# Optimization experiments

Measured on AMD Instinct MI355X. Metric: run time of the kernel, lower is better.

The kernel has to match this reference:

```python
import jax, jax.numpy as jnp
import numpy as np
import math
from jax import lax

B, C, L = 8, 512, 1024
NCONV, K, H = 4, 7, 8
DH = C // H
EPS = 1e-5
NEG = -1e30


def layer_norm(x, g, b):
    mu = jnp.mean(x, axis=-1, keepdims=True)
    var = jnp.mean(jnp.square(x - mu), axis=-1, keepdims=True)
    return (x - mu) * lax.rsqrt(var + EPS) * g + b


def positional_encoding(d, n):
    pos = jnp.arange(n, dtype=jnp.float32)[:, None]                     # [n,1]
    div = jnp.exp(jnp.arange(0, d, 2, dtype=jnp.float32) * (-math.log(10000.0) / d))
    ang = pos * div                                                      # [n,d/2]
    pe = jnp.zeros((d, n), dtype=jnp.float32)
    pe = pe.at[0::2].set(jnp.sin(ang).T).at[1::2].set(jnp.cos(ang).T)
    return pe                                                            # [d,n]


def setup_inputs() -> dict:
    key = jax.random.key(0)
    ks = jax.random.split(key, 20)
    s = 0.02
    inp = {
        "x": jax.random.normal(ks[0], (B, C, L), jnp.float32),
        "mask": jnp.ones((B, L), jnp.float32),
        # conv stack params (stacked over NCONV layers)
        "dw_w": jax.random.normal(ks[1], (NCONV, C, 1, K), jnp.float32) * s,
        "dw_b": jnp.zeros((NCONV, C), jnp.float32),
        "pw_w": jax.random.normal(ks[2], (NCONV, C, C), jnp.float32) * s,
        "pw_b": jnp.zeros((NCONV, C), jnp.float32),
        "ln_conv_g": jnp.ones((NCONV, C), jnp.float32),
        "ln_conv_b": jnp.zeros((NCONV, C), jnp.float32),
        # attention params (torch Linear layout: [out,in])
        "Wq": jax.random.normal(ks[3], (C, C), jnp.float32) * s,
        "bq": jnp.zeros((C,), jnp.float32),
        "Wk": jax.random.normal(ks[4], (C, C), jnp.float32) * s,
        "bk": jnp.zeros((C,), jnp.float32),
        "Wv": jax.random.normal(ks[5], (C, C), jnp.float32) * s,
        "bv": jnp.zeros((C,), jnp.float32),
        "Wo": jax.random.normal(ks[6], (C, C), jnp.float32) * s,
        "bo": jnp.zeros((C,), jnp.float32),
        "ln_att_g": jnp.ones((C,), jnp.float32),
        "ln_att_b": jnp.zeros((C,), jnp.float32),
        # final fc + its layernorm
        "Wf": jax.random.normal(ks[7], (C, C), jnp.float32) * s,
        "bf": jnp.zeros((C,), jnp.float32),
        "ln_fc_g": jnp.ones((C,), jnp.float32),
        "ln_fc_b": jnp.zeros((C,), jnp.float32),
    }
    return inp


def reference(x, mask, dw_w, dw_b, pw_w, pw_b, ln_conv_g, ln_conv_b,
              Wq, bq, Wk, bk, Wv, bv, Wo, bo, ln_att_g, ln_att_b,
              Wf, bf, ln_fc_g, ln_fc_b):
    # positional encoding on channels-first input, then -> [B,L,C]
    out = x + positional_encoding(C, L)[None]          # [B,C,L]; dropout = eval mode (identity)
    out = out.transpose(0, 2, 1)                       # [B,L,C]
    res = out
    for i in range(NCONV):                             # fixed small layer loop
        h = layer_norm(out, ln_conv_g[i], ln_conv_b[i])
        h = h.transpose(0, 2, 1)                       # [B,C,L]
        h = lax.conv_general_dilated(h, dw_w[i], (1,), [(K // 2, K // 2)],
                                     dimension_numbers=("NCH", "OIH", "NCH"),
                                     feature_group_count=C) + dw_b[i][None, :, None]
        h = jnp.einsum("bcl,oc->bol", h, pw_w[i]) + pw_b[i][None, :, None]
        h = jax.nn.relu(h).transpose(0, 2, 1)          # [B,L,C]
        out = h + res
        res = out
    # masked multi-head self-attention
    a = layer_norm(out, ln_att_g, ln_att_b)
    q = (a @ Wq.T + bq).reshape(B, L, H, DH)
    k = (a @ Wk.T + bk).reshape(B, L, H, DH)
    v = (a @ Wv.T + bv).reshape(B, L, H, DH)
    scale = 1.0 / math.sqrt(DH)
    scores = jnp.einsum("blhd,bmhd->bhlm", q, k) * scale   # [B,H,L,L]
    m = mask[:, None, None, :]                              # mask over keys
    scores = scores * m + (1.0 - m) * NEG
    attn = jax.nn.softmax(scores, axis=-1)
    o = jnp.einsum("bhlm,bmhd->blhd", attn, v).reshape(B, L, C)
    o = o @ Wo.T + bo
    out = o + res
    res = out
    # feed-forward (single Linear + relu) with residual
    f = layer_norm(out, ln_fc_g, ln_fc_b)
    f = jax.nn.relu(f @ Wf.T + bf)
    out = f + res
    return out
```

## Files before the change

kernel.cpp:

```cpp
#include <hip/hip_runtime.h>
#include <hip/hip_bf16.h>

#define L_SEQ 1024
#define CCH   512
#define NB    8

typedef __bf16 bf16_t;
typedef __bf16 bf16x4 __attribute__((ext_vector_type(4)));
typedef __bf16 bf16x8 __attribute__((ext_vector_type(8)));
typedef float  f32x4  __attribute__((ext_vector_type(4)));

__device__ __forceinline__ void gload_lds16(const void* g, void* l) {
  __builtin_amdgcn_global_load_lds((const __attribute__((address_space(1))) void*)g,
                                   (__attribute__((address_space(3))) void*)l, 16, 0, 0);
}

__global__ __launch_bounds__(256) void cvtall_kernel(
    const float* __restrict__ pw_w, const float* __restrict__ Wq,
    const float* __restrict__ Wk, const float* __restrict__ Wv,
    const float* __restrict__ Wo, const float* __restrict__ Wf,
    const float* __restrict__ dw_w,
    bf16_t* __restrict__ WPW, bf16_t* __restrict__ WQKV,
    bf16_t* __restrict__ WOB, bf16_t* __restrict__ WFB,
    float* __restrict__ WT) {
  int idx = blockIdx.x * 256 + threadIdx.x;
  if (idx < 1048576) { WPW[idx] = (bf16_t)pw_w[idx]; return; }
  idx -= 1048576;
  if (idx < 262144) { WQKV[idx] = (bf16_t)Wq[idx]; return; }
  idx -= 262144;
  if (idx < 262144) { WQKV[262144 + idx] = (bf16_t)Wk[idx]; return; }
  idx -= 262144;
  if (idx < 262144) { WQKV[524288 + idx] = (bf16_t)Wv[idx]; return; }
  idx -= 262144;
  if (idx < 262144) { WOB[idx] = (bf16_t)Wo[idx]; return; }
  idx -= 262144;
  if (idx < 262144) { WFB[idx] = (bf16_t)Wf[idx]; return; }
  idx -= 262144;
  if (idx < 14336) {
    int i = idx / 3584, r = idx % 3584, t = r >> 9, c = r & 511;
    WT[idx] = dw_w[i * 3584 + c * 7 + t];
  }
}

__global__ __launch_bounds__(256) void pet_kernel(float* __restrict__ PET) {
  int idx = blockIdx.x * 256 + threadIdx.x;
  int l = idx >> 9, c = idx & 511;
  float div = expf(-(float)(2 * (c >> 1)) * (9.210340371976184f / 512.0f));
  float ang = (float)l * div;
  PET[idx] = (c & 1) ? cosf(ang) : sinf(ang);
}

__global__ __launch_bounds__(256) void pe_kernel(const float* __restrict__ x,
                                                 const float* __restrict__ PET,
                                                 float* __restrict__ out) {
  __shared__ float tile[32][33];
  int l0 = blockIdx.x * 32, c0 = blockIdx.y * 32, b = blockIdx.z;
  int tx = threadIdx.x, ty = threadIdx.y;
#pragma unroll
  for (int r = 0; r < 32; r += 8)
    tile[ty + r][tx] = x[(size_t)(b * CCH + c0 + ty + r) * L_SEQ + l0 + tx];
  __syncthreads();
#pragma unroll
  for (int r = 0; r < 32; r += 8) {
    int l = l0 + ty + r, c = c0 + tx;
    out[(size_t)(b * L_SEQ + l) * CCH + c] = tile[tx][ty + r] + PET[l * CCH + c];
  }
}

__global__ __launch_bounds__(256) void stats_kernel(const float* __restrict__ in,
                                                    float* __restrict__ Psum,
                                                    float* __restrict__ Psq) {
  int w = threadIdx.x >> 6, l = threadIdx.x & 63;
  int row = blockIdx.x * 4 + w;
  const float* p = in + (size_t)row * CCH + l * 8;
  float v[8];
  *(float4*)(&v[0]) = *(const float4*)p;
  *(float4*)(&v[4]) = *(const float4*)(p + 4);
  float s = 0.f, q = 0.f;
#pragma unroll
  for (int j = 0; j < 8; j++) { s += v[j]; q += v[j] * v[j]; }
  s += __shfl_xor(s, 1); q += __shfl_xor(q, 1);
  s += __shfl_xor(s, 2); q += __shfl_xor(q, 2);
  s += __shfl_xor(s, 4); q += __shfl_xor(q, 4);
  if ((l & 7) == 0) {
    Psum[row * 8 + (l >> 3)] = s;
    Psq[row * 8 + (l >> 3)] = q;
  }
}

__global__ __launch_bounds__(256) void ln_apply_kernel(const float* __restrict__ in,
                                                       const float* __restrict__ Psum,
                                                       const float* __restrict__ Psq,
                                                       const float* __restrict__ gam,
                                                       const float* __restrict__ bet,
                                                       bf16_t* __restrict__ out) {
  int w = threadIdx.x >> 6, l = threadIdx.x & 63;
  int row = blockIdx.x * 4 + w;
  float v0 = 0.f;
  if (l < 8) v0 = Psum[row * 8 + l];
  else if (l < 16) v0 = Psq[row * 8 + (l - 8)];
  v0 += __shfl_xor(v0, 1); v0 += __shfl_xor(v0, 2); v0 += __shfl_xor(v0, 4);
  float sum = __shfl(v0, 0), sq = __shfl(v0, 8);
  float mean = sum * (1.0f / 512.0f);
  float var = sq * (1.0f / 512.0f) - mean * mean;
  float inv = rsqrtf(var + 1e-5f);
  const float* p = in + (size_t)row * CCH + l * 8;
  float v[8], gv[8], bv[8];
  *(float4*)(&v[0]) = *(const float4*)p;
  *(float4*)(&v[4]) = *(const float4*)(p + 4);
  *(float4*)(&gv[0]) = *(const float4*)(gam + l * 8);
  *(float4*)(&gv[4]) = *(const float4*)(gam + l * 8 + 4);
  *(float4*)(&bv[0]) = *(const float4*)(bet + l * 8);
  *(float4*)(&bv[4]) = *(const float4*)(bet + l * 8 + 4);
  bf16x8 o;
#pragma unroll
  for (int j = 0; j < 8; j++) o[j] = (bf16_t)((v[j] - mean) * inv * gv[j] + bv[j]);
  *(bf16x8*)(out + (size_t)row * CCH + l * 8) = o;
}

__global__ __launch_bounds__(256) void dwln_kernel(const float* __restrict__ in,
                                                   const float* __restrict__ Psum,
                                                   const float* __restrict__ Psq,
                                                   const float* __restrict__ gam,
                                                   const float* __restrict__ bet,
                                                   const float* __restrict__ wtt,
                                                   const float* __restrict__ dbias,
                                                   bf16_t* __restrict__ out) {
  int idx = blockIdx.x * 256 + threadIdx.x;
  int lane = threadIdx.x & 63;
  int row = idx >> 6;
  int l = row & (L_SEQ - 1);
  float m_ = 0.f, i_ = 0.f;
  if (lane < 7) {
    int ll = l + lane - 3;
    if (ll >= 0 && ll < L_SEQ) {
      int rr = row + lane - 3;
      float s = 0.f, q = 0.f;
#pragma unroll
      for (int c = 0; c < 8; c++) { s += Psum[rr * 8 + c]; q += Psq[rr * 8 + c]; }
      float mm = s * (1.0f / 512.0f);
      m_ = mm;
      i_ = rsqrtf(q * (1.0f / 512.0f) - mm * mm + 1e-5f);
    }
  }
  float gv[8], bv[8], acc[8];
  *(float4*)&gv[0] = *(const float4*)(gam + lane * 8);
  *(float4*)&gv[4] = *(const float4*)(gam + lane * 8 + 4);
  *(float4*)&bv[0] = *(const float4*)(bet + lane * 8);
  *(float4*)&bv[4] = *(const float4*)(bet + lane * 8 + 4);
  *(float4*)&acc[0] = *(const float4*)(dbias + lane * 8);
  *(float4*)&acc[4] = *(const float4*)(dbias + lane * 8 + 4);
#pragma unroll
  for (int t = 0; t < 7; t++) {
    float mt = __shfl(m_, t), it = __shfl(i_, t);
    int ll = l + t - 3;
    if (ll >= 0 && ll < L_SEQ) {
      const float* p = in + (size_t)(row + t - 3) * CCH + lane * 8;
      float v[8], wv[8];
      *(float4*)&v[0] = *(const float4*)p;
      *(float4*)&v[4] = *(const float4*)(p + 4);
      *(float4*)&wv[0] = *(const float4*)(wtt + t * CCH + lane * 8);
      *(float4*)&wv[4] = *(const float4*)(wtt + t * CCH + lane * 8 + 4);
#pragma unroll
      for (int j = 0; j < 8; j++)
        acc[j] += ((v[j] - mt) * it * gv[j] + bv[j]) * wv[j];
    }
  }
  bf16x8 o;
#pragma unroll
  for (int j = 0; j < 8; j++) o[j] = (bf16_t)acc[j];
  *(bf16x8*)&out[(size_t)row * CCH + lane * 8] = o;
}

#define GEMM_STAGE(SRCA, SRCB, BI, K0)                                            \
  do {                                                                            \
    _Pragma("unroll") for (int cc = 0; cc < 2; cc++) {                            \
      int row_ = cc * 32 + w * 8 + srow;                                          \
      int off_ = (scb ^ ((row_ & 7) << 4)) >> 1;                                  \
      gload_lds16(SRCA + (size_t)(m0 + row_) * CCH + (K0) + off_,                 \
                  &As[BI][(cc * 32 + w * 8) * 64]);                               \
    }                                                                             \
    _Pragma("unroll") for (int cc = 0; cc < 4; cc++) {                            \
      int row_ = cc * 32 + w * 8 + srow;                                          \
      int off_ = (scb ^ ((row_ & 7) << 4)) >> 1;                                  \
      gload_lds16(SRCB + (size_t)(n0 + row_) * CCH + (K0) + off_,                 \
                  &Bs[BI][(cc * 32 + w * 8) * 64]);                               \
    }                                                                             \
  } while (0)

#define GEMM_COMPUTE(BI)                                                          \
  do {                                                                            \
    _Pragma("unroll") for (int ks = 0; ks < 2; ks++) {                            \
      bf16x8 fa[2], fb[4];                                                        \
      _Pragma("unroll") for (int i = 0; i < 2; i++) {                             \
        int ra = wr * 32 + i * 16 + lc;                                           \
        fa[i] = *(const bf16x8*)&As[BI][ra * 64 +                                 \
                 (((ks * 64 + lg * 16) ^ ((ra & 7) << 4)) >> 1)];                 \
      }                                                                           \
      _Pragma("unroll") for (int j = 0; j < 4; j++) {                             \
        int rb = wc * 64 + j * 16 + lc;                                           \
        fb[j] = *(const bf16x8*)&Bs[BI][rb * 64 +                                 \
                 (((ks * 64 + lg * 16) ^ ((rb & 7) << 4)) >> 1)];                 \
      }                                                                           \
      _Pragma("unroll") for (int i = 0; i < 2; i++)                               \
        _Pragma("unroll") for (int j = 0; j < 4; j++)                             \
          acc[i][j] = __builtin_amdgcn_mfma_f32_16x16x32_bf16(fa[i], fb[j],       \
                                                              acc[i][j], 0, 0, 0);\
    }                                                                             \
  } while (0)

template <int RELU, int RES, int BF16OUT, int STATS>
__global__ __launch_bounds__(256) void gemm_kernel(const bf16_t* __restrict__ A,
                                                   const bf16_t* __restrict__ W,
                                                   const float* __restrict__ bias,
                                                   const float* __restrict__ res,
                                                   float* __restrict__ outf,
                                                   bf16_t* __restrict__ outb,
                                                   float* __restrict__ Psum,
                                                   float* __restrict__ Psq) {
  __shared__ __align__(16) bf16_t As[2][64 * 64];
  __shared__ __align__(16) bf16_t Bs[2][128 * 64];
  int tid = threadIdx.x;
  int w = tid >> 6, l = tid & 63;
  int m0 = blockIdx.x * 64, n0 = blockIdx.y * 128;
  int wr = w >> 1, wc = w & 1;
  int lc = l & 15, lg = l >> 4;
  int srow = l >> 3, scb = (l & 7) * 16;
  f32x4 acc[2][4];
#pragma unroll
  for (int i = 0; i < 2; i++)
#pragma unroll
    for (int j = 0; j < 4; j++) acc[i][j] = f32x4{0.f, 0.f, 0.f, 0.f};

  GEMM_STAGE(A, W, 0, 0);
  __syncthreads();
  int cur = 0;
  for (int t = 0; t < 8; t++) {
    if (t < 7) GEMM_STAGE(A, W, cur ^ 1, (t + 1) * 64);
    GEMM_COMPUTE(cur);
    __syncthreads();
    cur ^= 1;
  }

  float ps[2][4], pq[2][4];
  if (STATS) {
#pragma unroll
    for (int i = 0; i < 2; i++)
#pragma unroll
      for (int r = 0; r < 4; r++) { ps[i][r] = 0.f; pq[i][r] = 0.f; }
  }
#pragma unroll
  for (int i = 0; i < 2; i++) {
    int mbase = m0 + wr * 32 + i * 16 + lg * 4;
#pragma unroll
    for (int j = 0; j < 4; j++) {
      int n = n0 + wc * 64 + j * 16 + lc;
      float bn = bias[n];
#pragma unroll
      for (int r = 0; r < 4; r++) {
        int m = mbase + r;
        float v2 = acc[i][j][r] + bn;
        if (RELU) v2 = fmaxf(v2, 0.f);
        if (RES) v2 += res[(size_t)m * CCH + n];
        if (BF16OUT) outb[(size_t)m * CCH + n] = (bf16_t)v2;
        else outf[(size_t)m * CCH + n] = v2;
        if (STATS) { ps[i][r] += v2; pq[i][r] += v2 * v2; }
      }
    }
  }
  if (STATS) {
    int chunk = blockIdx.y * 2 + wc;
#pragma unroll
    for (int i = 0; i < 2; i++)
#pragma unroll
      for (int r = 0; r < 4; r++) {
        float s = ps[i][r], q = pq[i][r];
        s += __shfl_xor(s, 1); q += __shfl_xor(q, 1);
        s += __shfl_xor(s, 2); q += __shfl_xor(q, 2);
        s += __shfl_xor(s, 4); q += __shfl_xor(q, 4);
        s += __shfl_xor(s, 8); q += __shfl_xor(q, 8);
        if (lc == 0) {
          int row = m0 + wr * 32 + i * 16 + lg * 4 + r;
          Psum[row * 8 + chunk] = s;
          Psq[row * 8 + chunk] = q;
        }
      }
  }
}

__global__ __launch_bounds__(256) void qkv_kernel(const bf16_t* __restrict__ A,
                                                  const bf16_t* __restrict__ Wqkv,
                                                  const float* __restrict__ bq,
                                                  const float* __restrict__ bk,
                                                  const float* __restrict__ bv,
                                                  bf16_t* __restrict__ QB,
                                                  bf16_t* __restrict__ KB,
                                                  bf16_t* __restrict__ VT) {
  __shared__ __align__(16) bf16_t As[2][64 * 64];
  __shared__ __align__(16) bf16_t Bs[2][128 * 64];
  int tid = threadIdx.x;
  int w = tid >> 6, l = tid & 63;
  int m0 = blockIdx.x * 64, n0 = blockIdx.y * 128;
  int sec = n0 >> 9;
  int wr = w >> 1, wc = w & 1;
  int lc = l & 15, lg = l >> 4;
  int srow = l >> 3, scb = (l & 7) * 16;
  f32x4 acc[2][4];
#pragma unroll
  for (int i = 0; i < 2; i++)
#pragma unroll
    for (int j = 0; j < 4; j++) acc[i][j] = f32x4{0.f, 0.f, 0.f, 0.f};

  GEMM_STAGE(A, Wqkv, 0, 0);
  __syncthreads();
  int cur = 0;
  for (int t = 0; t < 8; t++) {
    if (t < 7) GEMM_STAGE(A, Wqkv, cur ^ 1, (t + 1) * 64);
    GEMM_COMPUTE(cur);
    __syncthreads();
    cur ^= 1;
  }

  const float* bp = (sec == 0) ? bq : (sec == 1) ? bk : bv;
#pragma unroll
  for (int i = 0; i < 2; i++) {
    int mbase = m0 + wr * 32 + i * 16 + lg * 4;
#pragma unroll
    for (int j = 0; j < 4; j++) {
      int n = n0 + wc * 64 + j * 16 + lc;
      int nl = n & 511;
      float bn = bp[nl];
      if (sec < 2) {
        bf16_t* ob = (sec == 0) ? QB : KB;
#pragma unroll
        for (int r = 0; r < 4; r++)
          ob[(size_t)(mbase + r) * CCH + nl] = (bf16_t)(acc[i][j][r] + bn);
      } else {
        int h = nl >> 6, d = nl & 63;
        int b = mbase >> 10, lpos = mbase & 1023;
        bf16x4 t;
#pragma unroll
        for (int r = 0; r < 4; r++) t[r] = (bf16_t)(acc[i][j][r] + bn);
        *(bf16x4*)&VT[(((size_t)(b * 8 + h) * 64 + d) * L_SEQ) + lpos] = t;
      }
    }
  }
}

__global__ __launch_bounds__(256) void attn_kernel(const bf16_t* __restrict__ Q,
                                                   const bf16_t* __restrict__ K,
                                                   const bf16_t* __restrict__ VT,
                                                   const float* __restrict__ mask,
                                                   bf16_t* __restrict__ O) {
  __shared__ __align__(16) bf16_t Ks[64 * 64];
  __shared__ __align__(16) bf16_t Vs[64 * 64];
  __shared__ __align__(16) bf16_t Pl[4][16 * 64];
  int tid = threadIdx.x;
  int w = tid >> 6, l = tid & 63;
  int bid = blockIdx.x;
  int sw = (bid & 7) * 128 + (bid >> 3);
  int qb = sw & 15, h = (sw >> 4) & 7, b = sw >> 7;
  int lg = l >> 4, lc = l & 15;

  int qrow = qb * 64 + w * 16 + lc;
  const bf16_t* qptr = Q + ((size_t)(b * L_SEQ + qrow) * CCH + h * 64);
  bf16x8 qf0 = *(const bf16x8*)(qptr + lg * 8);
  bf16x8 qf1 = *(const bf16x8*)(qptr + 32 + lg * 8);

  f32x4 oacc[4];
  float psl[4] = {0.f, 0.f, 0.f, 0.f};
#pragma unroll
  for (int nf = 0; nf < 4; nf++) oacc[nf] = f32x4{0.f, 0.f, 0.f, 0.f};

  int srow = l >> 3;
  int scb = (l & 7) * 16;

  for (int kc = 0; kc < 16; kc++) {
#pragma unroll
    for (int r = 0; r < 2; r++) {
      int row = r * 32 + w * 8 + srow;
      int sc = (scb ^ ((row & 7) << 4)) >> 1;
      int key = kc * 64 + row;
      gload_lds16(K + ((size_t)(b * L_SEQ + key) * CCH + h * 64 + sc),
                  &Ks[(r * 32 + w * 8) * 64]);
      gload_lds16(VT + (((size_t)(b * 8 + h) * 64 + row) * L_SEQ + kc * 64 + sc),
                  &Vs[(r * 32 + w * 8) * 64]);
    }
    __syncthreads();

    f32x4 sacc[4];
#pragma unroll
    for (int kf = 0; kf < 4; kf++) sacc[kf] = f32x4{0.f, 0.f, 0.f, 0.f};
#pragma unroll
    for (int kf = 0; kf < 4; kf++) {
      int row = kf * 16 + lc;
      int s = (row & 7) << 4;
      const bf16_t* kr = &Ks[row * 64];
      bf16x8 b0 = *(const bf16x8*)(kr + (((lg * 16) ^ s) >> 1));
      sacc[kf] = __builtin_amdgcn_mfma_f32_16x16x32_bf16(qf0, b0, sacc[kf], 0, 0, 0);
      bf16x8 b1 = *(const bf16x8*)(kr + (((64 + lg * 16) ^ s) >> 1));
      sacc[kf] = __builtin_amdgcn_mfma_f32_16x16x32_bf16(qf1, b1, sacc[kf], 0, 0, 0);
    }

#pragma unroll
    for (int kf = 0; kf < 4; kf++) {
      float mv = mask[b * L_SEQ + kc * 64 + kf * 16 + lc];
      float mneg = (1.f - mv) * (-1e30f);
      float msc = 0.125f * mv;
#pragma unroll
      for (int j = 0; j < 4; j++) {
        float p = __expf(sacc[kf][j] * msc + mneg);
        psl[j] += p;
        int q = lg * 4 + j;
        int cb = (kf * 32 + lc * 2) ^ ((q & 7) << 4);
        Pl[w][(q * 128 + cb) >> 1] = (bf16_t)p;
      }
    }

    int sp = (lc & 7) << 4;
    bf16x8 pa0 = *(const bf16x8*)&Pl[w][(lc * 128 + ((lg * 16) ^ sp)) >> 1];
    bf16x8 pa1 = *(const bf16x8*)&Pl[w][(lc * 128 + ((64 + lg * 16) ^ sp)) >> 1];
#pragma unroll
    for (int nf = 0; nf < 4; nf++) {
      int d = nf * 16 + lc;
      int s = (d & 7) << 4;
      const bf16_t* vr = &Vs[d * 64];
      bf16x8 vb0 = *(const bf16x8*)(vr + (((lg * 16) ^ s) >> 1));
      oacc[nf] = __builtin_amdgcn_mfma_f32_16x16x32_bf16(pa0, vb0, oacc[nf], 0, 0, 0);
      bf16x8 vb1 = *(const bf16x8*)(vr + (((64 + lg * 16) ^ s) >> 1));
      oacc[nf] = __builtin_amdgcn_mfma_f32_16x16x32_bf16(pa1, vb1, oacc[nf], 0, 0, 0);
    }
    __syncthreads();
  }

#pragma unroll
  for (int off = 1; off < 16; off <<= 1)
#pragma unroll
    for (int j = 0; j < 4; j++) psl[j] += __shfl_xor(psl[j], off);

#pragma unroll
  for (int j = 0; j < 4; j++) {
    float is = 1.0f / psl[j];
    int r = qb * 64 + w * 16 + lg * 4 + j;
    bf16_t* op = O + ((size_t)(b * L_SEQ + r) * CCH + h * 64);
#pragma unroll
    for (int nf = 0; nf < 4; nf++) op[nf * 16 + lc] = (bf16_t)(oacc[nf][j] * is);
  }
}

extern "C" void kernel_launch(void* const* d_in, const int* in_sizes, int n_in,
                              void* d_out, int out_size, void* d_ws, size_t ws_size,
                              hipStream_t stream) {
  const float* x = (const float*)d_in[0];
  const float* mask = (const float*)d_in[1];
  const float* dw_w = (const float*)d_in[2];
  const float* dw_b = (const float*)d_in[3];
  const float* pw_w = (const float*)d_in[4];
  const float* pw_b = (const float*)d_in[5];
  const float* ln_conv_g = (const float*)d_in[6];
  const float* ln_conv_b = (const float*)d_in[7];
  const float* Wq = (const float*)d_in[8];  const float* bq = (const float*)d_in[9];
  const float* Wk = (const float*)d_in[10]; const float* bk = (const float*)d_in[11];
  const float* Wv = (const float*)d_in[12]; const float* bv = (const float*)d_in[13];
  const float* Wo = (const float*)d_in[14]; const float* bo = (const float*)d_in[15];
  const float* ln_att_g = (const float*)d_in[16]; const float* ln_att_b = (const float*)d_in[17];
  const float* Wf = (const float*)d_in[18]; const float* bfc = (const float*)d_in[19];
  const float* ln_fc_g = (const float*)d_in[20]; const float* ln_fc_b = (const float*)d_in[21];

  float* OUT = (float*)d_out;

  char* ws = (char*)d_ws;
  bf16_t* ABF  = (bf16_t*)(ws);
  bf16_t* QB   = (bf16_t*)(ws + (8u << 20));
  bf16_t* KB   = (bf16_t*)(ws + (16u << 20));
  bf16_t* VT   = (bf16_t*)(ws + (24u << 20));
  char*   wb   = ws + (32u << 20);
  bf16_t* WPW  = (bf16_t*)(wb);
  bf16_t* WQKV = (bf16_t*)(wb + (2u << 20));
  bf16_t* WOB  = (bf16_t*)(wb + 3584u * 1024);
  bf16_t* WFB  = (bf16_t*)(wb + (4u << 20));
  float*  WT   = (float*)(wb + 4608u * 1024);
  float*  PET  = (float*)(ws + (37u << 20));
  float*  Psum = (float*)(ws + (39u << 20));
  float*  Psq  = (float*)(ws + (39u << 20) + 262144);

  cvtall_kernel<<<9272, 256, 0, stream>>>(pw_w, Wq, Wk, Wv, Wo, Wf, dw_w,
                                          WPW, WQKV, WOB, WFB, WT);
  pet_kernel<<<2048, 256, 0, stream>>>(PET);
  pe_kernel<<<dim3(32, 16, NB), dim3(32, 8), 0, stream>>>(x, PET, OUT);
  stats_kernel<<<2048, 256, 0, stream>>>(OUT, Psum, Psq);

  dim3 ggrid(128, 4);
  for (int i = 0; i < 4; i++) {
    dwln_kernel<<<2048, 256, 0, stream>>>(OUT, Psum, Psq, ln_conv_g + i * 512,
                                          ln_conv_b + i * 512, WT + i * 3584,
                                          dw_b + i * 512, ABF);
    gemm_kernel<1, 1, 0, 1><<<ggrid, 256, 0, stream>>>(ABF, WPW + i * 262144,
                                                       pw_b + i * 512, OUT, OUT,
                                                       nullptr, Psum, Psq);
  }
  ln_apply_kernel<<<2048, 256, 0, stream>>>(OUT, Psum, Psq, ln_att_g, ln_att_b, ABF);
  qkv_kernel<<<dim3(128, 12), 256, 0, stream>>>(ABF, WQKV, bq, bk, bv, QB, KB, VT);
  attn_kernel<<<1024, 256, 0, stream>>>(QB, KB, VT, mask, ABF);
  gemm_kernel<0, 1, 0, 1><<<ggrid, 256, 0, stream>>>(ABF, WOB, bo, OUT, OUT,
                                                     nullptr, Psum, Psq);
  ln_apply_kernel<<<2048, 256, 0, stream>>>(OUT, Psum, Psq, ln_fc_g, ln_fc_b, ABF);
  gemm_kernel<1, 1, 0, 0><<<ggrid, 256, 0, stream>>>(ABF, WFB, bfc, OUT,
                                                     (float*)d_out, nullptr,
                                                     nullptr, nullptr);
}
```

Measured before the change: 353.1 us.

## Process two query sub-tiles per attention block to reuse K/V tiles

Each attention block now handles 128 query rows (two 64-row sub-tiles) instead of 64. Every K/V tile staged into LDS is consumed twice, which halves global K/V traffic and barrier count per query row. The grid drops from 1024 to 512 blocks. s_setprio hints are also added around the MFMA sections. In exchange each thread holds more registers for the doubled accumulators, and the smaller grid may leave some compute units underused on a large GPU.

```diff
diff --git a/kernel.cpp b/kernel.cpp
--- a/kernel.cpp
+++ b/kernel.cpp
@@ -358,19 +358,28 @@
   int tid = threadIdx.x;
   int w = tid >> 6, l = tid & 63;
   int bid = blockIdx.x;
-  int sw = (bid & 7) * 128 + (bid >> 3);
-  int qb = sw & 15, h = (sw >> 4) & 7, b = sw >> 7;
+  int sw = (bid & 7) * 64 + (bid >> 3);
+  int qb = sw & 7, h = (sw >> 3) & 7, b = sw >> 6;
   int lg = l >> 4, lc = l & 15;
 
-  int qrow = qb * 64 + w * 16 + lc;
-  const bf16_t* qptr = Q + ((size_t)(b * L_SEQ + qrow) * CCH + h * 64);
-  bf16x8 qf0 = *(const bf16x8*)(qptr + lg * 8);
-  bf16x8 qf1 = *(const bf16x8*)(qptr + 32 + lg * 8);
-
-  f32x4 oacc[4];
-  float psl[4] = {0.f, 0.f, 0.f, 0.f};
-#pragma unroll
-  for (int nf = 0; nf < 4; nf++) oacc[nf] = f32x4{0.f, 0.f, 0.f, 0.f};
+  bf16x8 qf[2][2];
+#pragma unroll
+  for (int s = 0; s < 2; s++) {
+    int qrow = qb * 128 + s * 64 + w * 16 + lc;
+    const bf16_t* qptr = Q + ((size_t)(b * L_SEQ + qrow) * CCH + h * 64);
+    qf[s][0] = *(const bf16x8*)(qptr + lg * 8);
+    qf[s][1] = *(const bf16x8*)(qptr + 32 + lg * 8);
+  }
+
+  f32x4 oacc[2][4];
+  float psl[2][4];
+#pragma unroll
+  for (int s = 0; s < 2; s++)
+#pragma unroll
+    for (int nf = 0; nf < 4; nf++) {
+      oacc[s][nf] = f32x4{0.f, 0.f, 0.f, 0.f};
+      psl[s][nf] = 0.f;
+    }
 
   int srow = l >> 3;
   int scb = (l & 7) * 16;
@@ -388,47 +397,57 @@
     }
     __syncthreads();
 
-    f32x4 sacc[4];
-#pragma unroll
-    for (int kf = 0; kf < 4; kf++) sacc[kf] = f32x4{0.f, 0.f, 0.f, 0.f};
-#pragma unroll
-    for (int kf = 0; kf < 4; kf++) {
-      int row = kf * 16 + lc;
-      int s = (row & 7) << 4;
-      const bf16_t* kr = &Ks[row * 64];
-      bf16x8 b0 = *(const bf16x8*)(kr + (((lg * 16) ^ s) >> 1));
-      sacc[kf] = __builtin_amdgcn_mfma_f32_16x16x32_bf16(qf0, b0, sacc[kf], 0, 0, 0);
-      bf16x8 b1 = *(const bf16x8*)(kr + (((64 + lg * 16) ^ s) >> 1));
-      sacc[kf] = __builtin_amdgcn_mfma_f32_16x16x32_bf16(qf1, b1, sacc[kf], 0, 0, 0);
-    }
-
-#pragma unroll
-    for (int kf = 0; kf < 4; kf++) {
-      float mv = mask[b * L_SEQ + kc * 64 + kf * 16 + lc];
-      float mneg = (1.f - mv) * (-1e30f);
-      float msc = 0.125f * mv;
-#pragma unroll
-      for (int j = 0; j < 4; j++) {
-        float p = __expf(sacc[kf][j] * msc + mneg);
-        psl[j] += p;
-        int q = lg * 4 + j;
-        int cb = (kf * 32 + lc * 2) ^ ((q & 7) << 4);
-        Pl[w][(q * 128 + cb) >> 1] = (bf16_t)p;
+    float mv[4];
+#pragma unroll
+    for (int kf = 0; kf < 4; kf++) mv[kf] = mask[b * L_SEQ + kc * 64 + kf * 16 + lc];
+
+#pragma unroll
+    for (int s = 0; s < 2; s++) {
+      f32x4 sacc[4];
+#pragma unroll
+      for (int kf = 0; kf < 4; kf++) sacc[kf] = f32x4{0.f, 0.f, 0.f, 0.f};
+      __builtin_amdgcn_s_setprio(1);
+#pragma unroll
+      for (int kf = 0; kf < 4; kf++) {
+        int row = kf * 16 + lc;
+        int sx = (row & 7) << 4;
+        const bf16_t* kr = &Ks[row * 64];
+        bf16x8 b0 = *(const bf16x8*)(kr + (((lg * 16) ^ sx) >> 1));
+        sacc[kf] = __builtin_amdgcn_mfma_f32_16x16x32_bf16(qf[s][0], b0, sacc[kf], 0, 0, 0);
+        bf16x8 b1 = *(const bf16x8*)(kr + (((64 + lg * 16) ^ sx) >> 1));
+        sacc[kf] = __builtin_amdgcn_mfma_f32_16x16x32_bf16(qf[s][1], b1, sacc[kf], 0, 0, 0);
       }
-    }
-
-    int sp = (lc & 7) << 4;
-    bf16x8 pa0 = *(const bf16x8*)&Pl[w][(lc * 128 + ((lg * 16) ^ sp)) >> 1];
-    bf16x8 pa1 = *(const bf16x8*)&Pl[w][(lc * 128 + ((64 + lg * 16) ^ sp)) >> 1];
-#pragma unroll
-    for (int nf = 0; nf < 4; nf++) {
-      int d = nf * 16 + lc;
-      int s = (d & 7) << 4;
-      const bf16_t* vr = &Vs[d * 64];
-      bf16x8 vb0 = *(const bf16x8*)(vr + (((lg * 16) ^ s) >> 1));
-      oacc[nf] = __builtin_amdgcn_mfma_f32_16x16x32_bf16(pa0, vb0, oacc[nf], 0, 0, 0);
-      bf16x8 vb1 = *(const bf16x8*)(vr + (((64 + lg * 16) ^ s) >> 1));
-      oacc[nf] = __builtin_amdgcn_mfma_f32_16x16x32_bf16(pa1, vb1, oacc[nf], 0, 0, 0);
+      __builtin_amdgcn_s_setprio(0);
+
+#pragma unroll
+      for (int kf = 0; kf < 4; kf++) {
+        float mneg = (1.f - mv[kf]) * (-1e30f);
+        float msc = 0.125f * mv[kf];
+#pragma unroll
+        for (int j = 0; j < 4; j++) {
+          float p = __expf(sacc[kf][j] * msc + mneg);
+          psl[s][j] += p;
+          int q = lg * 4 + j;
+          int cb = (kf * 32 + lc * 2) ^ ((q & 7) << 4);
+          Pl[w][(q * 128 + cb) >> 1] = (bf16_t)p;
+        }
+      }
+
+      int sp = (lc & 7) << 4;
+      bf16x8 pa0 = *(const bf16x8*)&Pl[w][(lc * 128 + ((lg * 16) ^ sp)) >> 1];
+      bf16x8 pa1 = *(const bf16x8*)&Pl[w][(lc * 128 + ((64 + lg * 16) ^ sp)) >> 1];
+      __builtin_amdgcn_s_setprio(1);
+#pragma unroll
+      for (int nf = 0; nf < 4; nf++) {
+        int d = nf * 16 + lc;
+        int sx = (d & 7) << 4;
+        const bf16_t* vr = &Vs[d * 64];
+        bf16x8 vb0 = *(const bf16x8*)(vr + (((lg * 16) ^ sx) >> 1));
+        oacc[s][nf] = __builtin_amdgcn_mfma_f32_16x16x32_bf16(pa0, vb0, oacc[s][nf], 0, 0, 0);
+        bf16x8 vb1 = *(const bf16x8*)(vr + (((64 + lg * 16) ^ sx) >> 1));
+        oacc[s][nf] = __builtin_amdgcn_mfma_f32_16x16x32_bf16(pa1, vb1, oacc[s][nf], 0, 0, 0);
+      }
+      __builtin_amdgcn_s_setprio(0);
     }
     __syncthreads();
   }
@@ -436,16 +455,20 @@
 #pragma unroll
   for (int off = 1; off < 16; off <<= 1)
 #pragma unroll
-    for (int j = 0; j < 4; j++) psl[j] += __shfl_xor(psl[j], off);
-
-#pragma unroll
-  for (int j = 0; j < 4; j++) {
-    float is = 1.0f / psl[j];
-    int r = qb * 64 + w * 16 + lg * 4 + j;
-    bf16_t* op = O + ((size_t)(b * L_SEQ + r) * CCH + h * 64);
-#pragma unroll
-    for (int nf = 0; nf < 4; nf++) op[nf * 16 + lc] = (bf16_t)(oacc[nf][j] * is);
-  }
+    for (int s = 0; s < 2; s++)
+#pragma unroll
+      for (int j = 0; j < 4; j++) psl[s][j] += __shfl_xor(psl[s][j], off);
+
+#pragma unroll
+  for (int s = 0; s < 2; s++)
+#pragma unroll
+    for (int j = 0; j < 4; j++) {
+      float is = 1.0f / psl[s][j];
+      int r = qb * 128 + s * 64 + w * 16 + lg * 4 + j;
+      bf16_t* op = O + ((size_t)(b * L_SEQ + r) * CCH + h * 64);
+#pragma unroll
+      for (int nf = 0; nf < 4; nf++) op[nf * 16 + lc] = (bf16_t)(oacc[s][nf][j] * is);
+    }
 }
 
 extern "C" void kernel_launch(void* const* d_in, const int* in_sizes, int n_in,
@@ -501,7 +524,7 @@
   }
   ln_apply_kernel<<<2048, 256, 0, stream>>>(OUT, Psum, Psq, ln_att_g, ln_att_b, ABF);
   qkv_kernel<<<dim3(128, 12), 256, 0, stream>>>(ABF, WQKV, bq, bk, bv, QB, KB, VT);
-  attn_kernel<<<1024, 256, 0, stream>>>(QB, KB, VT, mask, ABF);
+  attn_kernel<<<512, 256, 0, stream>>>(QB, KB, VT, mask, ABF);
   gemm_kernel<0, 1, 0, 1><<<ggrid, 256, 0, stream>>>(ABF, WOB, bo, OUT, OUT,
                                                      nullptr, Psum, Psq);
   ln_apply_kernel<<<2048, 256, 0, stream>>>(OUT, Psum, Psq, ln_fc_g, ln_fc_b, ABF);
```

New measurement: 356.4 us. About the same (+0.9%).
